# Kernel optimization log

Measured on AMD Instinct MI355X. Metric: run time of the kernel, lower is better.

## Reference

```python
import jax, jax.numpy as jnp
import numpy as np

TOP_K = 2


def setup_inputs() -> dict:
    key = jax.random.key(0)
    ks = jax.random.split(key, 5)
    T, D, F, E = 2048, 2048, 7168, 8
    x = jax.random.normal(ks[0], (T, D), dtype=jnp.float32)
    gate_w = jax.random.normal(ks[1], (E, D), dtype=jnp.float32) * 0.02
    w1 = jax.random.normal(ks[2], (E, F, D), dtype=jnp.float32) * 0.02
    w3 = jax.random.normal(ks[3], (E, F, D), dtype=jnp.float32) * 0.02
    w2 = jax.random.normal(ks[4], (E, D, F), dtype=jnp.float32) * 0.02
    return {"x": x, "gate_w": gate_w, "w1": w1, "w3": w3, "w2": w2}


def reference(x, gate_w, w1, w3, w2):
    # x: (T, D); gate_w: (E, D); w1/w3: (E, F, D); w2: (E, D, F)
    T = x.shape[0]
    E = gate_w.shape[0]
    gate_logits = x @ gate_w.T                          # (T, E)
    all_probs = jax.nn.softmax(gate_logits.astype(jnp.float32), axis=-1)
    # keep only top-k probabilities (zero the rest), then renormalize
    top_vals, top_idx = jax.lax.top_k(all_probs, TOP_K)  # (T, k)
    rows = jnp.arange(T)[:, None]
    masked = jnp.zeros((T, E), dtype=jnp.float32).at[rows, top_idx].set(top_vals)
    weights = (masked / masked.sum(axis=1, keepdims=True)).astype(x.dtype)  # (T, E)
    # dense all-expert SwiGLU FFN, weighted accumulate
    g = jnp.einsum('td,efd->tef', x, w1)                # (T, E, F)
    u = jnp.einsum('td,efd->tef', x, w3)                # (T, E, F)
    h = jax.nn.silu(g) * u                              # (T, E, F)
    h = h * weights[:, :, None]
    out = jnp.einsum('tef,edf->td', h, w2)              # (T, D)
    return out
```

## Files before the change

kernel.cpp:

```cpp
#include <hip/hip_runtime.h>
#include <hip/hip_bf16.h>
#include <cstdint>
#include <cstddef>

#define TTOK 2048
#define DDIM 2048
#define FDIM 7168
#define NEXP 8
#define NMT (TTOK / 128)

typedef __attribute__((ext_vector_type(8))) short bf16x8;
typedef __attribute__((ext_vector_type(4))) float f32x4;

__device__ __forceinline__ unsigned short f2bf(float f) {
  __hip_bfloat16 h = __float2bfloat16(f);
  unsigned short s;
  __builtin_memcpy(&s, &h, 2);
  return s;
}

__device__ __forceinline__ ushort4 f2bf4(float4 v) {
  ushort4 o;
  o.x = f2bf(v.x); o.y = f2bf(v.y); o.z = f2bf(v.z); o.w = f2bf(v.w);
  return o;
}

__device__ __forceinline__ bf16x8 cvt8(f32x4 a, f32x4 b) {
  bf16x8 r;
  r[0] = (short)f2bf(a[0]); r[1] = (short)f2bf(a[1]);
  r[2] = (short)f2bf(a[2]); r[3] = (short)f2bf(a[3]);
  r[4] = (short)f2bf(b[0]); r[5] = (short)f2bf(b[1]);
  r[6] = (short)f2bf(b[2]); r[7] = (short)f2bf(b[3]);
  return r;
}

__device__ __forceinline__ void gload_lds16(const void* g, void* l) {
  __builtin_amdgcn_global_load_lds((const __attribute__((address_space(1))) void*)g,
                                   (__attribute__((address_space(3))) void*)l,
                                   16, 0, 0);
}

__global__ void cvt_x_kernel(const float* __restrict__ x, unsigned short* __restrict__ xb, int n4) {
  int i = blockIdx.x * blockDim.x + threadIdx.x;
  if (i >= n4) return;
  ((ushort4*)xb)[i] = f2bf4(((const float4*)x)[i]);
}

__global__ void gate_kernel(const float* __restrict__ x, const float* __restrict__ gw,
                            int* __restrict__ counts, int* __restrict__ lists,
                            float* __restrict__ wrow) {
  const int wv = threadIdx.x >> 6, ln = threadIdx.x & 63;
  const int t = blockIdx.x * 4 + wv;
  float acc[8];
  #pragma unroll
  for (int e = 0; e < 8; ++e) acc[e] = 0.f;
  const float* xp = x + (size_t)t * DDIM;
  for (int d = ln; d < DDIM; d += 64) {
    float xv = xp[d];
    #pragma unroll
    for (int e = 0; e < 8; ++e) acc[e] += xv * gw[e * DDIM + d];
  }
  #pragma unroll
  for (int e = 0; e < 8; ++e) {
    float v = acc[e];
    #pragma unroll
    for (int off = 32; off > 0; off >>= 1) v += __shfl_down(v, off);
    acc[e] = v;
  }
  if (ln == 0) {
    int i0 = 0;
    #pragma unroll
    for (int e = 1; e < 8; ++e) if (acc[e] > acc[i0]) i0 = e;
    int i1 = (i0 == 0) ? 1 : 0;
    #pragma unroll
    for (int e = 0; e < 8; ++e) if (e != i0 && acc[e] > acc[i1]) i1 = e;
    float p1 = expf(acc[i1] - acc[i0]);
    float w0 = 1.f / (1.f + p1);
    float w1v = p1 / (1.f + p1);
    int pos0 = atomicAdd(&counts[i0], 1);
    lists[i0 * TTOK + pos0] = t; wrow[i0 * TTOK + pos0] = w0;
    int pos1 = atomicAdd(&counts[i1], 1);
    lists[i1 * TTOK + pos1] = t; wrow[i1 * TTOK + pos1] = w1v;
  }
}

__global__ void prefix_kernel(const int* __restrict__ counts, int* __restrict__ hoff) {
  if (threadIdx.x == 0) {
    int s = 0;
    for (int e = 0; e < NEXP; ++e) { hoff[e] = s; s += counts[e]; }
  }
}


__launch_bounds__(256)
__global__ void gemm1f_kernel(const unsigned short* __restrict__ xb,
                              const float* __restrict__ w1,
                              const float* __restrict__ w3,
                              const int* __restrict__ counts,
                              const int* __restrict__ hoff,
                              const int* __restrict__ lists,
                              const float* __restrict__ wrow,
                              unsigned short* __restrict__ H) {
  const int ft = blockIdx.x, mt = blockIdx.y, e = blockIdx.z;
  const int cnt = counts[e];
  if (mt * 128 >= cnt) return;

  __shared__ __align__(16) unsigned short smA[128 * 32];
  __shared__ __align__(16) float smB1[128 * 32];
  __shared__ __align__(16) float smB3[128 * 32];
  __shared__ float smW[128];

  const int tid = threadIdx.x;
  const int wv = tid >> 6, ln = tid & 63;
  const int wr = wv >> 1, wc = wv & 1;

  if (tid < 128) {
    int pos = mt * 128 + tid;
    smW[tid] = (pos < cnt) ? wrow[e * TTOK + pos] : 0.f;
  }

  const int lcA = (tid & 3) ^ ((tid >> 3) & 3);
  const int* lst = lists + e * TTOK;
  const unsigned short* ap[2];
  #pragma unroll
  for (int q = 0; q < 2; ++q) {
    int pos = mt * 128 + q * 64 + (tid >> 2);
    int tok = (pos < cnt) ? lst[pos] : 0;
    ap[q] = xb + (size_t)tok * DDIM + lcA * 8;
  }

  const int lcB = (tid & 7) ^ ((tid >> 3) & 7);
  const size_t eoff = (size_t)e * FDIM * DDIM;
  const float* b1p[4];
  const float* b3p[4];
  #pragma unroll
  for (int q = 0; q < 4; ++q) {
    size_t row = (size_t)(ft * 128 + q * 32 + (tid >> 3));
    b1p[q] = w1 + eoff + row * DDIM + lcB * 4;
    b3p[q] = w3 + eoff + row * DDIM + lcB * 4;
  }

  f32x4 accG[4][4], accU[4][4];
  #pragma unroll
  for (int i = 0; i < 4; ++i)
    #pragma unroll
    for (int j = 0; j < 4; ++j) {
      accG[i][j] = (f32x4){0.f, 0.f, 0.f, 0.f};
      accU[i][j] = (f32x4){0.f, 0.f, 0.f, 0.f};
    }

  const int physA = ((ln >> 4) ^ ((ln >> 1) & 3)) * 8;
  const int physB0 = ((2 * (ln >> 4)) ^ (ln & 7)) * 4;
  const int physB1 = ((2 * (ln >> 4) + 1) ^ (ln & 7)) * 4;

  const int NKT = DDIM / 32;
  for (int kt = 0; kt < NKT; ++kt) {
    #pragma unroll
    for (int q = 0; q < 2; ++q)
      gload_lds16(ap[q] + kt * 32, (char*)smA + q * 4096 + tid * 16);
    #pragma unroll
    for (int q = 0; q < 4; ++q) {
      gload_lds16(b1p[q] + kt * 32, (char*)smB1 + q * 4096 + tid * 16);
      gload_lds16(b3p[q] + kt * 32, (char*)smB3 + q * 4096 + tid * 16);
    }
    __syncthreads();

    bf16x8 af[4], b1f[4], b3f[4];
    #pragma unroll
    for (int mi = 0; mi < 4; ++mi)
      af[mi] = *(const bf16x8*)(smA + (wr * 64 + mi * 16 + (ln & 15)) * 32 + physA);
    #pragma unroll
    for (int ni = 0; ni < 4; ++ni) {
      const int row = wc * 64 + ni * 16 + (ln & 15);
      f32x4 v0 = *(const f32x4*)(smB1 + row * 32 + physB0);
      f32x4 v1 = *(const f32x4*)(smB1 + row * 32 + physB1);
      b1f[ni] = cvt8(v0, v1);
      f32x4 u0 = *(const f32x4*)(smB3 + row * 32 + physB0);
      f32x4 u1 = *(const f32x4*)(smB3 + row * 32 + physB1);
      b3f[ni] = cvt8(u0, u1);
    }
    #pragma unroll
    for (int mi = 0; mi < 4; ++mi)
      #pragma unroll
      for (int ni = 0; ni < 4; ++ni) {
        accG[mi][ni] = __builtin_amdgcn_mfma_f32_16x16x32_bf16(af[mi], b1f[ni], accG[mi][ni], 0, 0, 0);
        accU[mi][ni] = __builtin_amdgcn_mfma_f32_16x16x32_bf16(af[mi], b3f[ni], accU[mi][ni], 0, 0, 0);
      }
    __syncthreads();
  }

  const int hbase = hoff[e];
  #pragma unroll
  for (int mi = 0; mi < 4; ++mi) {
    #pragma unroll
    for (int ni = 0; ni < 4; ++ni) {
      int col = ft * 128 + wc * 64 + ni * 16 + (ln & 15);
      #pragma unroll
      for (int r = 0; r < 4; ++r) {
        int rl = wr * 64 + mi * 16 + (ln >> 4) * 4 + r;
        int pos = mt * 128 + rl;
        if (pos < cnt) {
          float g = accG[mi][ni][r], u = accU[mi][ni][r];
          float s = g / (1.f + expf(-g));
          H[(size_t)(hbase + pos) * FDIM + col] = f2bf(s * u * smW[rl]);
        }
      }
    }
  }
}

__launch_bounds__(256)
__global__ void gemm2f_kernel(const unsigned short* __restrict__ H,
                              const float* __restrict__ w2,
                              const int* __restrict__ counts,
                              const int* __restrict__ hoff,
                              const int* __restrict__ lists,
                              float* __restrict__ out) {
  const int nt = blockIdx.x, e = blockIdx.z;
  const int mt = blockIdx.y >> 1, khalf = blockIdx.y & 1;
  const int cnt = counts[e];
  if (mt * 128 >= cnt) return;

  __shared__ __align__(16) unsigned short smA[128 * 32];
  __shared__ __align__(16) float smB[128 * 32];
  __shared__ int smTok[128];

  const int tid = threadIdx.x;
  const int wv = tid >> 6, ln = tid & 63;
  const int wr = wv >> 1, wc = wv & 1;

  if (tid < 128) {
    int pos = mt * 128 + tid;
    smTok[tid] = (pos < cnt) ? lists[e * TTOK + pos] : -1;
  }

  const int hbase = hoff[e];
  const int kofs = khalf * (FDIM / 2);

  const int lcA = (tid & 3) ^ ((tid >> 3) & 3);
  const unsigned short* ap[2];
  #pragma unroll
  for (int q = 0; q < 2; ++q)
    ap[q] = H + (size_t)(hbase + mt * 128 + q * 64 + (tid >> 2)) * FDIM + kofs + lcA * 8;

  const int lcB = (tid & 7) ^ ((tid >> 3) & 7);
  const float* bp[4];
  #pragma unroll
  for (int q = 0; q < 4; ++q)
    bp[q] = w2 + (size_t)e * DDIM * FDIM
               + (size_t)(nt * 128 + q * 32 + (tid >> 3)) * FDIM + kofs + lcB * 4;

  f32x4 acc[4][4];
  #pragma unroll
  for (int i = 0; i < 4; ++i)
    #pragma unroll
    for (int j = 0; j < 4; ++j) acc[i][j] = (f32x4){0.f, 0.f, 0.f, 0.f};

  const int physA = ((ln >> 4) ^ ((ln >> 1) & 3)) * 8;
  const int physB0 = ((2 * (ln >> 4)) ^ (ln & 7)) * 4;
  const int physB1 = ((2 * (ln >> 4) + 1) ^ (ln & 7)) * 4;

  const int NKT = (FDIM / 2) / 32;
  for (int kt = 0; kt < NKT; ++kt) {
    #pragma unroll
    for (int q = 0; q < 2; ++q)
      gload_lds16(ap[q] + kt * 32, (char*)smA + q * 4096 + tid * 16);
    #pragma unroll
    for (int q = 0; q < 4; ++q)
      gload_lds16(bp[q] + kt * 32, (char*)smB + q * 4096 + tid * 16);
    __syncthreads();

    bf16x8 af[4], bf[4];
    #pragma unroll
    for (int mi = 0; mi < 4; ++mi)
      af[mi] = *(const bf16x8*)(smA + (wr * 64 + mi * 16 + (ln & 15)) * 32 + physA);
    #pragma unroll
    for (int ni = 0; ni < 4; ++ni) {
      const int row = wc * 64 + ni * 16 + (ln & 15);
      f32x4 v0 = *(const f32x4*)(smB + row * 32 + physB0);
      f32x4 v1 = *(const f32x4*)(smB + row * 32 + physB1);
      bf[ni] = cvt8(v0, v1);
    }
    #pragma unroll
    for (int mi = 0; mi < 4; ++mi)
      #pragma unroll
      for (int ni = 0; ni < 4; ++ni)
        acc[mi][ni] = __builtin_amdgcn_mfma_f32_16x16x32_bf16(af[mi], bf[ni], acc[mi][ni], 0, 0, 0);
    __syncthreads();
  }

  #pragma unroll
  for (int mi = 0; mi < 4; ++mi) {
    #pragma unroll
    for (int ni = 0; ni < 4; ++ni) {
      int col = nt * 128 + wc * 64 + ni * 16 + (ln & 15);
      #pragma unroll
      for (int r = 0; r < 4; ++r) {
        int rl = wr * 64 + mi * 16 + (ln >> 4) * 4 + r;
        int tok = smTok[rl];
        if (tok >= 0) atomicAdd(out + (size_t)tok * DDIM + col, acc[mi][ni][r]);
      }
    }
  }
}

extern "C" void kernel_launch(void* const* d_in, const int* in_sizes, int n_in,
                              void* d_out, int out_size, void* d_ws, size_t ws_size,
                              hipStream_t stream) {
  const float* x  = (const float*)d_in[0];
  const float* gw = (const float*)d_in[1];
  const float* w1 = (const float*)d_in[2];
  const float* w3 = (const float*)d_in[3];
  const float* w2 = (const float*)d_in[4];
  float* out = (float*)d_out;
  char* ws = (char*)d_ws;

  const size_t XB_BYTES = (size_t)TTOK * DDIM * 2;
  const size_t H_BYTES  = (size_t)(2 * TTOK + 128) * FDIM * 2;

  unsigned short* xb = (unsigned short*)ws;
  unsigned short* H  = (unsigned short*)(ws + XB_BYTES);
  char* p = ws + XB_BYTES + H_BYTES;
  int*   lists  = (int*)p;          p += NEXP * TTOK * 4;
  float* wrow   = (float*)p;        p += NEXP * TTOK * 4;
  int*   counts = (int*)p;          p += 64;
  int*   hoff   = (int*)p;

  hipMemsetAsync(d_out, 0, (size_t)TTOK * DDIM * 4, stream);
  hipMemsetAsync(counts, 0, NEXP * 4, stream);

  cvt_x_kernel<<<(TTOK * DDIM / 4 + 255) / 256, 256, 0, stream>>>(x, xb, TTOK * DDIM / 4);
  gate_kernel<<<TTOK / 4, 256, 0, stream>>>(x, gw, counts, lists, wrow);
  prefix_kernel<<<1, 64, 0, stream>>>(counts, hoff);

  gemm1f_kernel<<<dim3(FDIM / 128, NMT, NEXP), 256, 0, stream>>>(
      xb, w1, w3, counts, hoff, lists, wrow, H);
  gemm2f_kernel<<<dim3(DDIM / 128, 2 * NMT, NEXP), 256, 0, stream>>>(
      H, w2, counts, hoff, lists, out);
}
```

Measured before the change: 1.341 ms.

## Double K-tile depth to 64 in both expert GEMMs and drop split-K in GEMM2

Both grouped GEMMs now stage K-tiles of 64 rather than 32 in LDS, with new XOR swizzles. Each barrier pair now covers two MFMA sub-steps, which halves the number of synchronisations and load rounds. GEMM2 no longer splits the F dimension across two blocks, so it does half as many output atomics but launches half as many blocks. Launch bounds request 2 blocks per CU. The larger LDS footprint (about 80KB in gemm1) may limit occupancy to one block per CU, which would conflict with that hint.

```diff
diff --git a/kernel.cpp b/kernel.cpp
--- a/kernel.cpp
+++ b/kernel.cpp
@@ -92,7 +92,7 @@
 }
 
 
-__launch_bounds__(256)
+__launch_bounds__(256, 2)
 __global__ void gemm1f_kernel(const unsigned short* __restrict__ xb,
                               const float* __restrict__ w1,
                               const float* __restrict__ w3,
@@ -105,9 +105,9 @@
   const int cnt = counts[e];
   if (mt * 128 >= cnt) return;
 
-  __shared__ __align__(16) unsigned short smA[128 * 32];
-  __shared__ __align__(16) float smB1[128 * 32];
-  __shared__ __align__(16) float smB3[128 * 32];
+  __shared__ __align__(16) unsigned short smA[128 * 64];
+  __shared__ __align__(16) float smB1[128 * 64];
+  __shared__ __align__(16) float smB3[128 * 64];
   __shared__ float smW[128];
 
   const int tid = threadIdx.x;
@@ -119,26 +119,21 @@
     smW[tid] = (pos < cnt) ? wrow[e * TTOK + pos] : 0.f;
   }
 
-  const int lcA = (tid & 3) ^ ((tid >> 3) & 3);
+  const int colSwz = (((ln & 7) ^ (ln >> 3)) * 8);
+  const int rlocal = wv * 8 + (ln >> 3);
   const int* lst = lists + e * TTOK;
-  const unsigned short* ap[2];
-  #pragma unroll
-  for (int q = 0; q < 2; ++q) {
-    int pos = mt * 128 + q * 64 + (tid >> 2);
+  const unsigned short* xap[4];
+  #pragma unroll
+  for (int q = 0; q < 4; ++q) {
+    int pos = mt * 128 + q * 32 + rlocal;
     int tok = (pos < cnt) ? lst[pos] : 0;
-    ap[q] = xb + (size_t)tok * DDIM + lcA * 8;
-  }
-
-  const int lcB = (tid & 7) ^ ((tid >> 3) & 7);
+    xap[q] = xb + (size_t)tok * DDIM + colSwz;
+  }
+
+  const int lcB = (tid & 15) ^ ((tid >> 4) & 15);
   const size_t eoff = (size_t)e * FDIM * DDIM;
-  const float* b1p[4];
-  const float* b3p[4];
-  #pragma unroll
-  for (int q = 0; q < 4; ++q) {
-    size_t row = (size_t)(ft * 128 + q * 32 + (tid >> 3));
-    b1p[q] = w1 + eoff + row * DDIM + lcB * 4;
-    b3p[q] = w3 + eoff + row * DDIM + lcB * 4;
-  }
+  const float* b1base = w1 + eoff + (size_t)(ft * 128 + (tid >> 4)) * DDIM + lcB * 4;
+  const float* b3base = w3 + eoff + (size_t)(ft * 128 + (tid >> 4)) * DDIM + lcB * 4;
 
   f32x4 accG[4][4], accU[4][4];
   #pragma unroll
@@ -149,43 +144,46 @@
       accU[i][j] = (f32x4){0.f, 0.f, 0.f, 0.f};
     }
 
-  const int physA = ((ln >> 4) ^ ((ln >> 1) & 3)) * 8;
-  const int physB0 = ((2 * (ln >> 4)) ^ (ln & 7)) * 4;
-  const int physB1 = ((2 * (ln >> 4) + 1) ^ (ln & 7)) * 4;
-
-  const int NKT = DDIM / 32;
+  const int NKT = DDIM / 64;
   for (int kt = 0; kt < NKT; ++kt) {
     #pragma unroll
-    for (int q = 0; q < 2; ++q)
-      gload_lds16(ap[q] + kt * 32, (char*)smA + q * 4096 + tid * 16);
-    #pragma unroll
-    for (int q = 0; q < 4; ++q) {
-      gload_lds16(b1p[q] + kt * 32, (char*)smB1 + q * 4096 + tid * 16);
-      gload_lds16(b3p[q] + kt * 32, (char*)smB3 + q * 4096 + tid * 16);
+    for (int q = 0; q < 4; ++q)
+      gload_lds16(xap[q] + kt * 64, (char*)smA + q * 4096 + wv * 1024);
+    #pragma unroll
+    for (int q = 0; q < 8; ++q) {
+      gload_lds16(b1base + (size_t)q * 16 * DDIM + kt * 64, (char*)smB1 + q * 4096 + tid * 16);
+      gload_lds16(b3base + (size_t)q * 16 * DDIM + kt * 64, (char*)smB3 + q * 4096 + tid * 16);
     }
     __syncthreads();
 
-    bf16x8 af[4], b1f[4], b3f[4];
-    #pragma unroll
-    for (int mi = 0; mi < 4; ++mi)
-      af[mi] = *(const bf16x8*)(smA + (wr * 64 + mi * 16 + (ln & 15)) * 32 + physA);
-    #pragma unroll
-    for (int ni = 0; ni < 4; ++ni) {
-      const int row = wc * 64 + ni * 16 + (ln & 15);
-      f32x4 v0 = *(const f32x4*)(smB1 + row * 32 + physB0);
-      f32x4 v1 = *(const f32x4*)(smB1 + row * 32 + physB1);
-      b1f[ni] = cvt8(v0, v1);
-      f32x4 u0 = *(const f32x4*)(smB3 + row * 32 + physB0);
-      f32x4 u1 = *(const f32x4*)(smB3 + row * 32 + physB1);
-      b3f[ni] = cvt8(u0, u1);
-    }
-    #pragma unroll
-    for (int mi = 0; mi < 4; ++mi)
+    #pragma unroll
+    for (int kk = 0; kk < 2; ++kk) {
+      const int physA = ((kk * 4 + (ln >> 4)) ^ (ln & 7)) * 8;
+      const int c0 = kk * 8 + (ln >> 4) * 2;
+      bf16x8 af[4], b1f[4], b3f[4];
+      #pragma unroll
+      for (int mi = 0; mi < 4; ++mi)
+        af[mi] = *(const bf16x8*)(smA + (wr * 64 + mi * 16 + (ln & 15)) * 64 + physA);
       #pragma unroll
       for (int ni = 0; ni < 4; ++ni) {
-        accG[mi][ni] = __builtin_amdgcn_mfma_f32_16x16x32_bf16(af[mi], b1f[ni], accG[mi][ni], 0, 0, 0);
-        accU[mi][ni] = __builtin_amdgcn_mfma_f32_16x16x32_bf16(af[mi], b3f[ni], accU[mi][ni], 0, 0, 0);
+        const int row = wc * 64 + ni * 16 + (ln & 15);
+        const int p0 = (c0 ^ (row & 15)) * 4;
+        const int p1 = ((c0 + 1) ^ (row & 15)) * 4;
+        f32x4 a0 = *(const f32x4*)(smB1 + row * 64 + p0);
+        f32x4 a1 = *(const f32x4*)(smB1 + row * 64 + p1);
+        b1f[ni] = cvt8(a0, a1);
+        f32x4 c0v = *(const f32x4*)(smB3 + row * 64 + p0);
+        f32x4 c1v = *(const f32x4*)(smB3 + row * 64 + p1);
+        b3f[ni] = cvt8(c0v, c1v);
       }
+      #pragma unroll
+      for (int mi = 0; mi < 4; ++mi)
+        #pragma unroll
+        for (int ni = 0; ni < 4; ++ni) {
+          accG[mi][ni] = __builtin_amdgcn_mfma_f32_16x16x32_bf16(af[mi], b1f[ni], accG[mi][ni], 0, 0, 0);
+          accU[mi][ni] = __builtin_amdgcn_mfma_f32_16x16x32_bf16(af[mi], b3f[ni], accU[mi][ni], 0, 0, 0);
+        }
+    }
     __syncthreads();
   }
 
@@ -209,20 +207,19 @@
   }
 }
 
-__launch_bounds__(256)
+__launch_bounds__(256, 2)
 __global__ void gemm2f_kernel(const unsigned short* __restrict__ H,
                               const float* __restrict__ w2,
                               const int* __restrict__ counts,
                               const int* __restrict__ hoff,
                               const int* __restrict__ lists,
                               float* __restrict__ out) {
-  const int nt = blockIdx.x, e = blockIdx.z;
-  const int mt = blockIdx.y >> 1, khalf = blockIdx.y & 1;
+  const int nt = blockIdx.x, mt = blockIdx.y, e = blockIdx.z;
   const int cnt = counts[e];
   if (mt * 128 >= cnt) return;
 
-  __shared__ __align__(16) unsigned short smA[128 * 32];
-  __shared__ __align__(16) float smB[128 * 32];
+  __shared__ __align__(16) unsigned short smA[128 * 64];
+  __shared__ __align__(16) float smB[128 * 64];
   __shared__ int smTok[128];
 
   const int tid = threadIdx.x;
@@ -234,21 +231,18 @@
     smTok[tid] = (pos < cnt) ? lists[e * TTOK + pos] : -1;
   }
 
+  const int colSwz = (((ln & 7) ^ (ln >> 3)) * 8);
+  const int rlocal = wv * 8 + (ln >> 3);
   const int hbase = hoff[e];
-  const int kofs = khalf * (FDIM / 2);
-
-  const int lcA = (tid & 3) ^ ((tid >> 3) & 3);
-  const unsigned short* ap[2];
-  #pragma unroll
-  for (int q = 0; q < 2; ++q)
-    ap[q] = H + (size_t)(hbase + mt * 128 + q * 64 + (tid >> 2)) * FDIM + kofs + lcA * 8;
-
-  const int lcB = (tid & 7) ^ ((tid >> 3) & 7);
-  const float* bp[4];
+
+  const unsigned short* hap[4];
   #pragma unroll
   for (int q = 0; q < 4; ++q)
-    bp[q] = w2 + (size_t)e * DDIM * FDIM
-               + (size_t)(nt * 128 + q * 32 + (tid >> 3)) * FDIM + kofs + lcB * 4;
+    hap[q] = H + (size_t)(hbase + mt * 128 + q * 32 + rlocal) * FDIM + colSwz;
+
+  const int lcB = (tid & 15) ^ ((tid >> 4) & 15);
+  const float* b2base = w2 + (size_t)e * DDIM * FDIM
+                           + (size_t)(nt * 128 + (tid >> 4)) * FDIM + lcB * 4;
 
   f32x4 acc[4][4];
   #pragma unroll
@@ -256,36 +250,39 @@
     #pragma unroll
     for (int j = 0; j < 4; ++j) acc[i][j] = (f32x4){0.f, 0.f, 0.f, 0.f};
 
-  const int physA = ((ln >> 4) ^ ((ln >> 1) & 3)) * 8;
-  const int physB0 = ((2 * (ln >> 4)) ^ (ln & 7)) * 4;
-  const int physB1 = ((2 * (ln >> 4) + 1) ^ (ln & 7)) * 4;
-
-  const int NKT = (FDIM / 2) / 32;
+  const int NKT = FDIM / 64;
   for (int kt = 0; kt < NKT; ++kt) {
     #pragma unroll
-    for (int q = 0; q < 2; ++q)
-      gload_lds16(ap[q] + kt * 32, (char*)smA + q * 4096 + tid * 16);
-    #pragma unroll
     for (int q = 0; q < 4; ++q)
-      gload_lds16(bp[q] + kt * 32, (char*)smB + q * 4096 + tid * 16);
+      gload_lds16(hap[q] + kt * 64, (char*)smA + q * 4096 + wv * 1024);
+    #pragma unroll
+    for (int q = 0; q < 8; ++q)
+      gload_lds16(b2base + (size_t)q * 16 * FDIM + kt * 64, (char*)smB + q * 4096 + tid * 16);
     __syncthreads();
 
-    bf16x8 af[4], bf[4];
-    #pragma unroll
-    for (int mi = 0; mi < 4; ++mi)
-      af[mi] = *(const bf16x8*)(smA + (wr * 64 + mi * 16 + (ln & 15)) * 32 + physA);
-    #pragma unroll
-    for (int ni = 0; ni < 4; ++ni) {
-      const int row = wc * 64 + ni * 16 + (ln & 15);
-      f32x4 v0 = *(const f32x4*)(smB + row * 32 + physB0);
-      f32x4 v1 = *(const f32x4*)(smB + row * 32 + physB1);
-      bf[ni] = cvt8(v0, v1);
-    }
-    #pragma unroll
-    for (int mi = 0; mi < 4; ++mi)
-      #pragma unroll
-      for (int ni = 0; ni < 4; ++ni)
-        acc[mi][ni] = __builtin_amdgcn_mfma_f32_16x16x32_bf16(af[mi], bf[ni], acc[mi][ni], 0, 0, 0);
+    #pragma unroll
+    for (int kk = 0; kk < 2; ++kk) {
+      const int physA = ((kk * 4 + (ln >> 4)) ^ (ln & 7)) * 8;
+      const int c0 = kk * 8 + (ln >> 4) * 2;
+      bf16x8 af[4], bf[4];
+      #pragma unroll
+      for (int mi = 0; mi < 4; ++mi)
+        af[mi] = *(const bf16x8*)(smA + (wr * 64 + mi * 16 + (ln & 15)) * 64 + physA);
+      #pragma unroll
+      for (int ni = 0; ni < 4; ++ni) {
+        const int row = wc * 64 + ni * 16 + (ln & 15);
+        const int p0 = (c0 ^ (row & 15)) * 4;
+        const int p1 = ((c0 + 1) ^ (row & 15)) * 4;
+        f32x4 v0 = *(const f32x4*)(smB + row * 64 + p0);
+        f32x4 v1 = *(const f32x4*)(smB + row * 64 + p1);
+        bf[ni] = cvt8(v0, v1);
+      }
+      #pragma unroll
+      for (int mi = 0; mi < 4; ++mi)
+        #pragma unroll
+        for (int ni = 0; ni < 4; ++ni)
+          acc[mi][ni] = __builtin_amdgcn_mfma_f32_16x16x32_bf16(af[mi], bf[ni], acc[mi][ni], 0, 0, 0);
+    }
     __syncthreads();
   }
 
@@ -335,6 +332,6 @@
 
   gemm1f_kernel<<<dim3(FDIM / 128, NMT, NEXP), 256, 0, stream>>>(
       xb, w1, w3, counts, hoff, lists, wrow, H);
-  gemm2f_kernel<<<dim3(DDIM / 128, 2 * NMT, NEXP), 256, 0, stream>>>(
+  gemm2f_kernel<<<dim3(DDIM / 128, NMT, NEXP), 256, 0, stream>>>(
       H, w2, counts, hoff, lists, out);
 }
```

After: 1.132 ms. 15.6% less time.
